# Kernel optimization log

Measured on AMD Instinct MI355X. Metric: run time of the kernel, lower is better.

Reference implementation:

```python
import jax, jax.numpy as jnp
import numpy as np

EPS = 1e-8
V_LAMBDA = 1.0
T_LAMBDA = 1.0
BB, DIM = 8192, 256


def _rowwise_cos(a, b):
    # torch.cosine_similarity semantics: dot / (max(|a|,eps) * max(|b|,eps))
    na = jnp.maximum(jnp.linalg.norm(a, axis=-1), EPS)
    nb = jnp.maximum(jnp.linalg.norm(b, axis=-1), EPS)
    return jnp.sum(a * b, axis=-1) / (na * nb)


def _clamped_normalize(x):
    n = jnp.maximum(jnp.linalg.norm(x, axis=-1, keepdims=True), EPS)
    return x / n


def _retrieval_acc(sim, labels):
    # sim: [v, t]; top-1 retrieval accuracy in percent
    return jnp.mean((jnp.argmax(sim, axis=-1) == labels).astype(jnp.float32)) * 100.0


def setup_inputs() -> dict:
    key = jax.random.key(0)
    ks = jax.random.split(key, 5)
    names = ['vis_pred', 'text_pred', 'vis_feats_proj', 'caption_emb', 'vis_feats_proj_narr']
    return {n: jax.random.normal(k, (BB, DIM), dtype=jnp.float32) for n, k in zip(names, ks)}


def reference(vis_pred, text_pred, vis_feats_proj, caption_emb, vis_feats_proj_narr):
    bb = vis_pred.shape[0]
    labels = jnp.arange(bb)

    # training losses (row-wise cosine similarity)
    vis_loss = jnp.mean(1.0 - _rowwise_cos(vis_pred, vis_feats_proj))
    text_loss = jnp.mean(1.0 - _rowwise_cos(text_pred, caption_emb))
    loss = V_LAMBDA * vis_loss + T_LAMBDA * text_loss

    # retrieval accuracies (no_grad block). The torch repeat_interleave/repeat +
    # elementwise cosine construction is exactly the pairwise cosine-sim matrix:
    # normalize rows once, then a [bb, dim] x [dim, bb] GEMM.
    v = _clamped_normalize(jax.lax.stop_gradient(vis_pred))
    gt_v = _clamped_normalize(jax.lax.stop_gradient(vis_feats_proj))
    narr_v = _clamped_normalize(jax.lax.stop_gradient(vis_feats_proj_narr))
    gt_t = _clamped_normalize(jax.lax.stop_gradient(caption_emb))
    # NOTE: in the original code both t_r and gt_t_r are tiles of gt_text, so
    # the 'text' side of every sim matrix is gt_t. We reproduce that faithfully.

    acc_gtv_gtt = _retrieval_acc(jnp.einsum('vd,td->vt', gt_v, gt_t), labels)
    acc_v_gtt = _retrieval_acc(jnp.einsum('vd,td->vt', v, gt_t), labels)
    acc_gtv_t = _retrieval_acc(jnp.einsum('vd,td->vt', gt_v, gt_t), labels)
    acc_v_t = _retrieval_acc(jnp.einsum('vd,td->vt', v, gt_t), labels)
    acc_narr_gtt = _retrieval_acc(jnp.einsum('vd,td->vt', narr_v, gt_t), labels)
    acc_narr_t = _retrieval_acc(jnp.einsum('vd,td->vt', narr_v, gt_t), labels)

    # order: vis_loss, text_loss, loss, gt_v-gt_t, v-gt_t, gt_v-t, v-t, narr_v-gt_t, narr_v-t
    return jnp.stack([vis_loss, text_loss, loss,
                      acc_gtv_gtt, acc_v_gtt, acc_gtv_t, acc_v_t,
                      acc_narr_gtt, acc_narr_t])
```

## Files before the change

kernel.cpp:

```cpp
#include <hip/hip_runtime.h>
#include <hip/hip_bf16.h>
#include <stdint.h>
#include <limits.h>

#define BB 8192
#define DIM 256

typedef __attribute__((ext_vector_type(4))) int int32x4;

__device__ __forceinline__ void load_lds16(const char* g, char* l) {
  __builtin_amdgcn_global_load_lds(
      (const __attribute__((address_space(1))) unsigned int*)g,
      (__attribute__((address_space(3))) unsigned int*)l, 16, 0, 0);
}

__device__ __forceinline__ float q8f(float x) {
  return rintf(fmaxf(fminf(x * 256.f, 127.f), -127.f));
}

__device__ __forceinline__ int dpp_max16(int u) {
  int t;
  t = __builtin_amdgcn_update_dpp(0, u, 0xB1, 0xF, 0xF, true);
  u = t > u ? t : u;
  t = __builtin_amdgcn_update_dpp(0, u, 0x4E, 0xF, 0xF, true);
  u = t > u ? t : u;
  t = __builtin_amdgcn_update_dpp(0, u, 0x124, 0xF, 0xF, true);
  u = t > u ? t : u;
  t = __builtin_amdgcn_update_dpp(0, u, 0x128, 0xF, 0xF, true);
  u = t > u ? t : u;
  return u;
}

__global__ __launch_bounds__(256) void phase1(
    const float* __restrict__ vp,  const float* __restrict__ tp,
    const float* __restrict__ vfp, const float* __restrict__ ce,
    const float* __restrict__ nr,
    float* __restrict__ rowcos, int* __restrict__ diag,
    char* __restrict__ vbuf, char* __restrict__ gvbuf,
    char* __restrict__ nvbuf, char* __restrict__ gtbuf,
    int* __restrict__ maxComb, float* __restrict__ sums,
    int* __restrict__ ticket) {
  const int wave = threadIdx.x >> 6;
  const int lane = threadIdx.x & 63;
  const int row  = blockIdx.x * 4 + wave;
  const int base = row * DIM + lane * 4;

  float4 a = *(const float4*)&vp[base];
  float4 t = *(const float4*)&tp[base];
  float4 g = *(const float4*)&vfp[base];
  float4 c = *(const float4*)&ce[base];
  float4 n = *(const float4*)&nr[base];

  float s[7];
  s[0] = a.x*a.x + a.y*a.y + a.z*a.z + a.w*a.w;
  s[1] = g.x*g.x + g.y*g.y + g.z*g.z + g.w*g.w;
  s[2] = a.x*g.x + a.y*g.y + a.z*g.z + a.w*g.w;
  s[3] = t.x*t.x + t.y*t.y + t.z*t.z + t.w*t.w;
  s[4] = c.x*c.x + c.y*c.y + c.z*c.z + c.w*c.w;
  s[5] = t.x*c.x + t.y*c.y + t.z*c.z + t.w*c.w;
  s[6] = n.x*n.x + n.y*n.y + n.z*n.z + n.w*n.w;

  #pragma unroll
  for (int mk = 1; mk < 64; mk <<= 1) {
    #pragma unroll
    for (int q = 0; q < 7; ++q) s[q] += __shfl_xor(s[q], mk);
  }

  const float eps = 1e-8f;
  float na = fmaxf(sqrtf(s[0]), eps);
  float ng = fmaxf(sqrtf(s[1]), eps);
  float nt = fmaxf(sqrtf(s[3]), eps);
  float nc = fmaxf(sqrtf(s[4]), eps);
  float nn = fmaxf(sqrtf(s[6]), eps);
  float ia = 1.f / na, ig = 1.f / ng, ic = 1.f / nc, in_ = 1.f / nn;

  float qa0 = q8f(a.x*ia), qa1 = q8f(a.y*ia), qa2 = q8f(a.z*ia), qa3 = q8f(a.w*ia);
  float qg0 = q8f(g.x*ig), qg1 = q8f(g.y*ig), qg2 = q8f(g.z*ig), qg3 = q8f(g.w*ig);
  float qn0 = q8f(n.x*in_), qn1 = q8f(n.y*in_), qn2 = q8f(n.z*in_), qn3 = q8f(n.w*in_);
  float qc0 = q8f(c.x*ic), qc1 = q8f(c.y*ic), qc2 = q8f(c.z*ic), qc3 = q8f(c.w*ic);

  float d[3];
  d[0] = qg0*qc0 + qg1*qc1 + qg2*qc2 + qg3*qc3;
  d[1] = qa0*qc0 + qa1*qc1 + qa2*qc2 + qa3*qc3;
  d[2] = qn0*qc0 + qn1*qc1 + qn2*qc2 + qn3*qc3;
  #pragma unroll
  for (int mk = 1; mk < 64; mk <<= 1) {
    #pragma unroll
    for (int q = 0; q < 3; ++q) d[q] += __shfl_xor(d[q], mk);
  }

  auto pack = [](float x0, float x1, float x2, float x3) -> unsigned {
    return ((unsigned)((int)x0 & 0xFF)) | ((unsigned)((int)x1 & 0xFF) << 8) |
           ((unsigned)((int)x2 & 0xFF) << 16) | ((unsigned)((int)x3 & 0xFF) << 24);
  };
  int idx = row * 64 + lane;
  ((unsigned*)vbuf)[idx]  = pack(qa0, qa1, qa2, qa3);
  ((unsigned*)gvbuf)[idx] = pack(qg0, qg1, qg2, qg3);
  ((unsigned*)nvbuf)[idx] = pack(qn0, qn1, qn2, qn3);
  ((unsigned*)gtbuf)[idx] = pack(qc0, qc1, qc2, qc3);

  if (lane == 0) {
    rowcos[row]      = s[2] / (na * ng);
    rowcos[BB + row] = s[5] / (nt * nc);
    diag[0 * BB + row] = (int)d[0];
    diag[1 * BB + row] = (int)d[1];
    diag[2 * BB + row] = (int)d[2];
    maxComb[0 * BB + row] = INT_MIN;
    maxComb[1 * BB + row] = INT_MIN;
    maxComb[2 * BB + row] = INT_MIN;
  }
  if (blockIdx.x == 0 && threadIdx.x < 5) sums[threadIdx.x] = 0.f;
  if (blockIdx.x == 0 && threadIdx.x == 5) *ticket = 0;
}

__global__ __launch_bounds__(256, 4) void sim_argmax(
    const char* __restrict__ Abase, const char* __restrict__ B,
    int* __restrict__ maxComb) {
  __shared__ char As[128 * 128];
  __shared__ char Bs[128 * 128];
  __shared__ int comb[128][2];

  const int tid  = threadIdx.x;
  const int lane = tid & 63;
  const int wave = tid >> 6;
  const int wr   = wave >> 1, wc = wave & 1;
  const int m    = lane & 15, quad = lane >> 4;
  const int z    = blockIdx.z;

  const int rowTile = blockIdx.y * 128;
  const int colTile = blockIdx.x * 128;
  const char* A  = Abase + (size_t)z * BB * DIM + (size_t)rowTile * DIM;
  const char* Bp = B + (size_t)colTile * DIM;

  int32x4 acc[4][4];
  #pragma unroll
  for (int i = 0; i < 4; ++i)
    #pragma unroll
    for (int j = 0; j < 4; ++j) acc[i][j] = (int32x4){0, 0, 0, 0};

  int offs[4];
  #pragma unroll
  for (int t = 0; t < 4; ++t) {
    int c   = t * 256 + tid;
    int row = c >> 3;
    int l   = (c & 7) ^ (row & 7);
    offs[t] = row * DIM + l * 16;
  }

  #pragma unroll
  for (int s = 0; s < 2; ++s) {
    if (s) __syncthreads();
    #pragma unroll
    for (int t = 0; t < 4; ++t) {
      const int c = t * 256 + tid;
      load_lds16(&A[offs[t] + s * 128],  &As[c * 16]);
      load_lds16(&Bp[offs[t] + s * 128], &Bs[c * 16]);
    }
    __syncthreads();

    #pragma unroll
    for (int kp = 0; kp < 2; ++kp) {
      int32x4 af[4], bf[4];
      #pragma unroll
      for (int rt = 0; rt < 4; ++rt) {
        int ar = wr * 64 + rt * 16 + m;
        int p  = (kp * 4 + quad) ^ (m & 7);
        af[rt] = *(const int32x4*)&As[ar * 128 + p * 16];
      }
      #pragma unroll
      for (int ct = 0; ct < 4; ++ct) {
        int br = wc * 64 + ct * 16 + m;
        int p  = (kp * 4 + quad) ^ (m & 7);
        bf[ct] = *(const int32x4*)&Bs[br * 128 + p * 16];
      }
      #pragma unroll
      for (int rt = 0; rt < 4; ++rt)
        #pragma unroll
        for (int ct = 0; ct < 4; ++ct)
          acc[rt][ct] = __builtin_amdgcn_mfma_i32_16x16x64_i8(
              af[rt], bf[ct], acc[rt][ct], 0, 0, 0);
    }
  }

  const int rowBase = rowTile + wr * 64;
  const int colBase = colTile + wc * 64;
  #pragma unroll
  for (int rt = 0; rt < 4; ++rt) {
    #pragma unroll
    for (int reg = 0; reg < 4; ++reg) {
      int i = rowBase + rt * 16 + quad * 4 + reg;
      int u = INT_MIN;
      #pragma unroll
      for (int ct = 0; ct < 4; ++ct) {
        int j = colBase + ct * 16 + m;
        int w = acc[rt][ct][reg] * 2 + ((j < i) ? 1 : 0);
        w = (j == i) ? INT_MIN : w;
        u = (w > u) ? w : u;
      }
      u = dpp_max16(u);
      if (m == 0) comb[wr * 64 + rt * 16 + quad * 4 + reg][wc] = u;
    }
  }
  __syncthreads();
  if (tid < 128) {
    int u0 = comb[tid][0], u1 = comb[tid][1];
    atomicMax(&maxComb[(size_t)z * BB + rowTile + tid], u0 > u1 ? u0 : u1);
  }
}

__global__ __launch_bounds__(256) void phase3_fin(
    const int* __restrict__ diag, const int* __restrict__ maxComb,
    const float* __restrict__ rowcos,
    float* __restrict__ sums, int* __restrict__ ticket,
    float* __restrict__ out) {
  __shared__ float red[4][5];
  __shared__ bool amLast;
  int r = blockIdx.x * 256 + threadIdx.x;
  int lane = threadIdx.x & 63, wave = threadIdx.x >> 6;
  float v[5];
  v[0] = rowcos[r];
  v[1] = rowcos[BB + r];
  #pragma unroll
  for (int z = 0; z < 3; ++z)
    v[2 + z] = (2 * diag[z * BB + r] >= maxComb[z * BB + r]) ? 1.f : 0.f;
  #pragma unroll
  for (int mk = 1; mk < 64; mk <<= 1) {
    #pragma unroll
    for (int q = 0; q < 5; ++q) v[q] += __shfl_xor(v[q], mk);
  }
  if (lane == 0) {
    #pragma unroll
    for (int q = 0; q < 5; ++q) red[wave][q] = v[q];
  }
  __syncthreads();
  if (threadIdx.x < 5) {
    float acc = red[0][threadIdx.x] + red[1][threadIdx.x] +
                red[2][threadIdx.x] + red[3][threadIdx.x];
    atomicAdd(&sums[threadIdx.x], acc);
  }
  __threadfence();
  __syncthreads();
  if (threadIdx.x == 0)
    amLast = (atomicAdd(ticket, 1) == (int)gridDim.x - 1);
  __syncthreads();
  if (amLast && threadIdx.x == 0) {
    float s0 = atomicAdd(&sums[0], 0.f);
    float s1 = atomicAdd(&sums[1], 0.f);
    float s2 = atomicAdd(&sums[2], 0.f);
    float s3 = atomicAdd(&sums[3], 0.f);
    float s4 = atomicAdd(&sums[4], 0.f);
    float vl = 1.f - s0 * (1.f / BB);
    float tl = 1.f - s1 * (1.f / BB);
    out[0] = vl;
    out[1] = tl;
    out[2] = vl + tl;
    float a0 = s2 * (100.f / BB);
    float a1 = s3 * (100.f / BB);
    float a2 = s4 * (100.f / BB);
    out[3] = a0;
    out[4] = a1;
    out[5] = a0;
    out[6] = a1;
    out[7] = a2;
    out[8] = a2;
  }
}

extern "C" void kernel_launch(void* const* d_in, const int* in_sizes, int n_in,
                              void* d_out, int out_size, void* d_ws, size_t ws_size,
                              hipStream_t stream) {
  const float* vp  = (const float*)d_in[0];
  const float* tp  = (const float*)d_in[1];
  const float* vfp = (const float*)d_in[2];
  const float* ce  = (const float*)d_in[3];
  const float* nr  = (const float*)d_in[4];

  char* ws = (char*)d_ws;
  float* sums    = (float*)ws;
  int*   ticket  = (int*)(ws + 32);
  int*   maxComb = (int*)(ws + 64);
  int*   diag    = maxComb + 3 * BB;
  float* rowcos  = (float*)(diag + 3 * BB);
  char*  gvbuf   = (char*)(rowcos + 2 * BB);
  char*  vbuf    = gvbuf + (size_t)BB * DIM;
  char*  nvbuf   = vbuf  + (size_t)BB * DIM;
  char*  gtbuf   = nvbuf + (size_t)BB * DIM;


  phase1<<<BB / 4, 256, 0, stream>>>(vp, tp, vfp, ce, nr, rowcos, diag,
                                     vbuf, gvbuf, nvbuf, gtbuf, maxComb, sums,
                                     ticket);

  dim3 grid(BB / 128, BB / 128, 3);
  sim_argmax<<<grid, 256, 0, stream>>>(gvbuf, gtbuf, maxComb);

  phase3_fin<<<BB / 256, 256, 0, stream>>>(diag, maxComb, rowcos, sums, ticket,
                                           (float*)d_out);
}
```

Before: 164.2 us.

## Pre-swizzle A operands into MFMA fragment layout and load them directly to registers

Phase1 now writes the three quantized A matrices (gt_v, v, narr_v) through LDS into a fragment-major layout, so each wave's MFMA A-fragments sit contiguously in global memory. The GEMM kernel then loads A fragments straight into registers with a one-step prefetch and stages only the B tile in LDS, taking the full 256-wide K in one pass with a 16-way XOR swizzle. This removes A staging through LDS and one of the two sync rounds. In exchange each block re-reads A from global or L2 without sharing, and LDS use per block rises from 32KB to 33KB-plus for B.

Measured after the change: 159.3 us. 1.03x faster.

```diff
diff --git a/kernel.cpp b/kernel.cpp
--- a/kernel.cpp
+++ b/kernel.cpp
@@ -36,10 +36,11 @@
     const float* __restrict__ vfp, const float* __restrict__ ce,
     const float* __restrict__ nr,
     float* __restrict__ rowcos, int* __restrict__ diag,
-    char* __restrict__ vbuf, char* __restrict__ gvbuf,
-    char* __restrict__ nvbuf, char* __restrict__ gtbuf,
+    char* __restrict__ abuf,
+    char* __restrict__ gtbuf,
     int* __restrict__ maxComb, float* __restrict__ sums,
     int* __restrict__ ticket) {
+  __shared__ unsigned ldsT[3][4][64];
   const int wave = threadIdx.x >> 6;
   const int lane = threadIdx.x & 63;
   const int row  = blockIdx.x * 4 + wave;
@@ -74,10 +75,10 @@
   float nn = fmaxf(sqrtf(s[6]), eps);
   float ia = 1.f / na, ig = 1.f / ng, ic = 1.f / nc, in_ = 1.f / nn;
 
-  float qa0 = q8f(a.x*ia), qa1 = q8f(a.y*ia), qa2 = q8f(a.z*ia), qa3 = q8f(a.w*ia);
-  float qg0 = q8f(g.x*ig), qg1 = q8f(g.y*ig), qg2 = q8f(g.z*ig), qg3 = q8f(g.w*ig);
-  float qn0 = q8f(n.x*in_), qn1 = q8f(n.y*in_), qn2 = q8f(n.z*in_), qn3 = q8f(n.w*in_);
-  float qc0 = q8f(c.x*ic), qc1 = q8f(c.y*ic), qc2 = q8f(c.z*ic), qc3 = q8f(c.w*ic);
+  float qa0=q8f(a.x*ia), qa1=q8f(a.y*ia), qa2=q8f(a.z*ia), qa3=q8f(a.w*ia);
+  float qg0=q8f(g.x*ig), qg1=q8f(g.y*ig), qg2=q8f(g.z*ig), qg3=q8f(g.w*ig);
+  float qn0=q8f(n.x*in_),qn1=q8f(n.y*in_),qn2=q8f(n.z*in_),qn3=q8f(n.w*in_);
+  float qc0=q8f(c.x*ic), qc1=q8f(c.y*ic), qc2=q8f(c.z*ic), qc3=q8f(c.w*ic);
 
   float d[3];
   d[0] = qg0*qc0 + qg1*qc1 + qg2*qc2 + qg3*qc3;
@@ -93,15 +94,14 @@
     return ((unsigned)((int)x0 & 0xFF)) | ((unsigned)((int)x1 & 0xFF) << 8) |
            ((unsigned)((int)x2 & 0xFF) << 16) | ((unsigned)((int)x3 & 0xFF) << 24);
   };
-  int idx = row * 64 + lane;
-  ((unsigned*)vbuf)[idx]  = pack(qa0, qa1, qa2, qa3);
-  ((unsigned*)gvbuf)[idx] = pack(qg0, qg1, qg2, qg3);
-  ((unsigned*)nvbuf)[idx] = pack(qn0, qn1, qn2, qn3);
-  ((unsigned*)gtbuf)[idx] = pack(qc0, qc1, qc2, qc3);
+  ((unsigned*)gtbuf)[row * 64 + lane] = pack(qc0, qc1, qc2, qc3);
+  ldsT[0][wave][lane] = pack(qg0, qg1, qg2, qg3);
+  ldsT[1][wave][lane] = pack(qa0, qa1, qa2, qa3);
+  ldsT[2][wave][lane] = pack(qn0, qn1, qn2, qn3);
 
   if (lane == 0) {
-    rowcos[row]      = s[2] / (na * ng);
-    rowcos[BB + row] = s[5] / (nt * nc);
+    rowcos[row]        = s[2] / (na * ng);
+    rowcos[BB + row]   = s[5] / (nt * nc);
     diag[0 * BB + row] = (int)d[0];
     diag[1 * BB + row] = (int)d[1];
     diag[2 * BB + row] = (int)d[2];
@@ -111,13 +111,22 @@
   }
   if (blockIdx.x == 0 && threadIdx.x < 5) sums[threadIdx.x] = 0.f;
   if (blockIdx.x == 0 && threadIdx.x == 5) *ticket = 0;
+
+  __syncthreads();
+  if (threadIdx.x < 192) {
+    int mat = threadIdx.x >> 6, l = threadIdx.x & 63;
+    int kc = l >> 2, j = l & 3;
+    uint4 val = *(const uint4*)&ldsT[mat][j][kc * 4];
+    int tileR = blockIdx.x >> 2;
+    int rm    = (blockIdx.x & 3) * 4 + j;
+    *(uint4*)&abuf[(size_t)mat * BB * DIM + tileR * 4096 + kc * 256 + rm * 16] = val;
+  }
 }
 
 __global__ __launch_bounds__(256, 4) void sim_argmax(
-    const char* __restrict__ Abase, const char* __restrict__ B,
+    const char* __restrict__ Af, const char* __restrict__ B,
     int* __restrict__ maxComb) {
-  __shared__ char As[128 * 128];
-  __shared__ char Bs[128 * 128];
+  __shared__ char Bs[128 * 256];
   __shared__ int comb[128][2];
 
   const int tid  = threadIdx.x;
@@ -129,57 +138,54 @@
 
   const int rowTile = blockIdx.y * 128;
   const int colTile = blockIdx.x * 128;
-  const char* A  = Abase + (size_t)z * BB * DIM + (size_t)rowTile * DIM;
+  const char* Az = Af + (size_t)z * BB * DIM + (size_t)(rowTile >> 4) * 4096;
   const char* Bp = B + (size_t)colTile * DIM;
 
+  #pragma unroll
+  for (int t = 0; t < 8; ++t) {
+    const int c   = t * 256 + tid;
+    const int row = c >> 4;
+    const int l   = (c & 15) ^ (row & 15);
+    load_lds16(&Bp[row * DIM + l * 16], &Bs[c * 16]);
+  }
+
   int32x4 acc[4][4];
   #pragma unroll
   for (int i = 0; i < 4; ++i)
     #pragma unroll
     for (int j = 0; j < 4; ++j) acc[i][j] = (int32x4){0, 0, 0, 0};
 
-  int offs[4];
-  #pragma unroll
-  for (int t = 0; t < 4; ++t) {
-    int c   = t * 256 + tid;
-    int row = c >> 3;
-    int l   = (c & 7) ^ (row & 7);
-    offs[t] = row * DIM + l * 16;
-  }
-
-  #pragma unroll
-  for (int s = 0; s < 2; ++s) {
-    if (s) __syncthreads();
-    #pragma unroll
-    for (int t = 0; t < 4; ++t) {
-      const int c = t * 256 + tid;
-      load_lds16(&A[offs[t] + s * 128],  &As[c * 16]);
-      load_lds16(&Bp[offs[t] + s * 128], &Bs[c * 16]);
-    }
-    __syncthreads();
-
-    #pragma unroll
-    for (int kp = 0; kp < 2; ++kp) {
-      int32x4 af[4], bf[4];
-      #pragma unroll
-      for (int rt = 0; rt < 4; ++rt) {
-        int ar = wr * 64 + rt * 16 + m;
-        int p  = (kp * 4 + quad) ^ (m & 7);
-        af[rt] = *(const int32x4*)&As[ar * 128 + p * 16];
-      }
-      #pragma unroll
-      for (int ct = 0; ct < 4; ++ct) {
-        int br = wc * 64 + ct * 16 + m;
-        int p  = (kp * 4 + quad) ^ (m & 7);
-        bf[ct] = *(const int32x4*)&Bs[br * 128 + p * 16];
-      }
+  int32x4 af[4];
+  #pragma unroll
+  for (int rt = 0; rt < 4; ++rt)
+    af[rt] = *(const int32x4*)&Az[(size_t)(wr * 4 + rt) * 4096 + lane * 16];
+
+  __syncthreads();
+
+  #pragma unroll
+  for (int kp = 0; kp < 4; ++kp) {
+    int32x4 a[4];
+    #pragma unroll
+    for (int rt = 0; rt < 4; ++rt) a[rt] = af[rt];
+    if (kp < 3) {
       #pragma unroll
       for (int rt = 0; rt < 4; ++rt)
-        #pragma unroll
-        for (int ct = 0; ct < 4; ++ct)
-          acc[rt][ct] = __builtin_amdgcn_mfma_i32_16x16x64_i8(
-              af[rt], bf[ct], acc[rt][ct], 0, 0, 0);
+        af[rt] = *(const int32x4*)&Az[(size_t)(wr * 4 + rt) * 4096 +
+                                      (kp + 1) * 1024 + lane * 16];
     }
+    int32x4 bf[4];
+    #pragma unroll
+    for (int ct = 0; ct < 4; ++ct) {
+      int br = wc * 64 + ct * 16 + m;
+      int p  = (kp * 4 + quad) ^ m;
+      bf[ct] = *(const int32x4*)&Bs[br * 256 + p * 16];
+    }
+    #pragma unroll
+    for (int rt = 0; rt < 4; ++rt)
+      #pragma unroll
+      for (int ct = 0; ct < 4; ++ct)
+        acc[rt][ct] = __builtin_amdgcn_mfma_i32_16x16x64_i8(
+            a[rt], bf[ct], acc[rt][ct], 0, 0, 0);
   }
 
   const int rowBase = rowTile + wr * 64;
@@ -281,18 +287,15 @@
   int*   maxComb = (int*)(ws + 64);
   int*   diag    = maxComb + 3 * BB;
   float* rowcos  = (float*)(diag + 3 * BB);
-  char*  gvbuf   = (char*)(rowcos + 2 * BB);
-  char*  vbuf    = gvbuf + (size_t)BB * DIM;
-  char*  nvbuf   = vbuf  + (size_t)BB * DIM;
-  char*  gtbuf   = nvbuf + (size_t)BB * DIM;
+  char*  abuf    = (char*)(rowcos + 2 * BB);
+  char*  gtbuf   = abuf + (size_t)3 * BB * DIM;
 
 
   phase1<<<BB / 4, 256, 0, stream>>>(vp, tp, vfp, ce, nr, rowcos, diag,
-                                     vbuf, gvbuf, nvbuf, gtbuf, maxComb, sums,
-                                     ticket);
+                                     abuf, gtbuf, maxComb, sums, ticket);
 
   dim3 grid(BB / 128, BB / 128, 3);
-  sim_argmax<<<grid, 256, 0, stream>>>(gvbuf, gtbuf, maxComb);
+  sim_argmax<<<grid, 256, 0, stream>>>(abuf, gtbuf, maxComb);
 
   phase3_fin<<<BB / 256, 256, 0, stream>>>(diag, maxComb, rowcos, sums, ticket,
                                            (float*)d_out);
```
